# Optimization experiments

Hardware: AMD Instinct MI355X
Metric: run time of the kernel (lower is better)

## Reference

```python
import jax, jax.numpy as jnp
import numpy as np

B, S, D = 4, 4096, 256


def setup_inputs() -> dict:
    key = jax.random.key(0)
    k1, k2, k3 = jax.random.split(key, 3)
    x = jax.random.normal(k1, (B, S, D), dtype=jnp.float32)
    w_int = jax.random.randint(k2, (D, D), 0, 127, dtype=jnp.int32)  # quantized weight (out, in)
    scale = jax.random.uniform(k3, (D,), dtype=jnp.float32)          # per-output-channel scale
    return {"x": x, "w_int": w_int, "scale": scale}


def reference(x, w_int, scale):
    # self-attention: q = k = v = x, single head over feature dim D
    inv_sqrt_d = 1.0 / jnp.sqrt(jnp.asarray(D, dtype=x.dtype))
    scores = jnp.einsum('bqd,bkd->bqk', x, x) * inv_sqrt_d   # [B,S,S]
    probs = jax.nn.softmax(scores, axis=-1)
    attn = jnp.einsum('bqk,bkd->bqd', probs, x)              # [B,S,D]
    # quantized linear: dequantize then matmul (y = attn @ W^T)
    W = w_int.astype(x.dtype) * scale[:, None]               # [D_out, D_in]
    return jnp.einsum('bsd,od->bso', attn, W)
```

## Files before the change

### kernel.cpp

```cpp
#include <hip/hip_runtime.h>

typedef __bf16 bf16x8 __attribute__((ext_vector_type(8)));
typedef float f32x16 __attribute__((ext_vector_type(16)));
typedef unsigned short u16x8 __attribute__((ext_vector_type(8)));

constexpr int B = 4, S = 4096, D = 256;
constexpr float CSC = 0.09016844005556021f;

static __device__ __forceinline__ unsigned short f2bf(float f) {
  unsigned int u = __builtin_bit_cast(unsigned int, f);
  u = (u + 0x7fffu + ((u >> 16) & 1u)) >> 16;
  return (unsigned short)u;
}

static __device__ __forceinline__ float bf2f(unsigned short u) {
  unsigned int v = ((unsigned int)u) << 16;
  return __builtin_bit_cast(float, v);
}

static __device__ __forceinline__ unsigned int pk2bf(float lo, float hi) {
  unsigned int r;
  asm("v_cvt_pk_bf16_f32 %0, %1, %2" : "=v"(r) : "v"(lo), "v"(hi));
  return r;
}

static __device__ __forceinline__ void gld16(const void* g, void* l) {
  __builtin_amdgcn_global_load_lds(
      (const __attribute__((address_space(1))) unsigned int*)g,
      (__attribute__((address_space(3))) unsigned int*)l, 16, 0, 0);
}

#define FENCE_LGKM()                                          \
  do {                                                        \
    asm volatile("s_waitcnt lgkmcnt(0)" ::: "memory");        \
    __builtin_amdgcn_s_barrier();                             \
    asm volatile("" ::: "memory");                            \
  } while (0)
#define FENCE_ALL()                                               \
  do {                                                            \
    asm volatile("s_waitcnt vmcnt(0) lgkmcnt(0)" ::: "memory");   \
    __builtin_amdgcn_s_barrier();                                 \
    asm volatile("" ::: "memory");                                \
  } while (0)

__global__ __launch_bounds__(256) void k_prep(const float* __restrict__ x,
                                              unsigned short* __restrict__ xbf,
                                              unsigned short* __restrict__ xK,
                                              unsigned short* __restrict__ xV) {
  __shared__ unsigned short T[64][72];
  __shared__ unsigned short R[64][72];
  int bid = blockIdx.x;
  int b = bid >> 8, rem = bid & 255;
  int s0 = (rem >> 2) * 64, d0 = (rem & 3) * 64;
  int j = threadIdx.x & 63, i0 = threadIdx.x >> 6;
#pragma unroll
  for (int k = 0; k < 16; ++k) {
    int i = k * 4 + i0;
    int idx = (b * S + s0 + i) * D + d0 + j;
    unsigned short v = f2bf(x[idx]);
    xbf[idx] = v;
    T[j][i] = v;
    R[i][j] = v;
  }
  __syncthreads();
  int t = s0 >> 6;
#pragma unroll
  for (int p = 0; p < 2; ++p) {
    int cc = p * 256 + threadIdx.x;
    int i = cc >> 3;
    int sl = (cc >> 1) & 3;
    int half = cc & 1;
    u16x8 v = *(const u16x8*)&R[i][sl * 16 + half * 8];
    int s = (d0 >> 4) + sl;
    *(u16x8*)((char*)xK + (size_t)((b * 64 + t) * 16 + s) * 2048 + i * 32 + half * 16) = v;
  }
#pragma unroll
  for (int p = 0; p < 2; ++p) {
    int cc = p * 256 + threadIdx.x;
    int dl = cc >> 3;
    int p8 = cc & 7;
    u16x8 v = *(const u16x8*)&T[dl][p8 * 8];
    int c = p8 >> 1;
    *(u16x8*)((char*)xV + (size_t)((b * 64 + t) * 4 + c) * 8192 + (d0 + dl) * 32 +
              (p8 & 1) * 16) = v;
  }
}

__global__ __launch_bounds__(256) void k_deqw(const int* __restrict__ w,
                                              unsigned short* __restrict__ wbf) {
  int i = blockIdx.x * 256 + threadIdx.x;
  wbf[i] = f2bf((float)w[i]);
}

__global__ __launch_bounds__(512, 2) void k_attn(const unsigned short* __restrict__ xbf,
                                                 const unsigned short* __restrict__ xK,
                                                 const unsigned short* __restrict__ xV,
                                                 unsigned short* __restrict__ PO0,
                                                 unsigned short* __restrict__ PO1,
                                                 float* __restrict__ ML) {
  __shared__ __align__(16) char smem[147456];

  int tid = threadIdx.x;
  int w = tid >> 6, lane = tid & 63;
  int q5 = lane & 31, hi = lane >> 5;
  int pair = w >> 1, dh = w & 1;

  int bid = blockIdx.x;
  int swz = (bid & 7) * 32 + (bid >> 3);
  int h = swz & 1;
  int qg = swz >> 1;
  int q0 = qg * 128;
  int bat = q0 >> 12;
  int qloc = q0 & (S - 1);

  const unsigned short* Xb = xbf + (size_t)bat * (S * D);
  int qw = qloc + pair * 32;
  int koff = q5 * 32 + hi * 16;

  bf16x8 qf[16];
#pragma unroll
  for (int s = 0; s < 16; ++s)
    qf[s] = *(const bf16x8*)(Xb + (qw + q5) * D + s * 16 + hi * 8);

  f32x16 acc[4];
#pragma unroll
  for (int dt = 0; dt < 4; ++dt)
#pragma unroll
    for (int j = 0; j < 16; ++j) acc[dt][j] = 0.f;
  float l_lane = 0.f;

  const char* xKb = (const char*)xK + (size_t)(bat * 64 + h * 32) * 32768;
  const char* xVb = (const char*)xV + (size_t)(bat * 64 + h * 32) * 32768;

  auto STAGE = [&](int itile, int bb) {
    char* Kd = smem + bb * 32768;
    char* Vd = smem + 65536 + bb * 32768;
    const char* srcK = xKb + (size_t)itile * 32768;
    const char* srcV = xVb + (size_t)itile * 32768;
#pragma unroll
    for (int i = 0; i < 4; ++i) {
      int off = (w * 2 + (i >> 1)) * 2048 + (i & 1) * 1024;
      gld16(srcK + off + lane * 16, Kd + off);
    }
#pragma unroll
    for (int i = 0; i < 4; ++i) {
      int off = (w >> 1) * 8192 + ((w & 1) * 4 + i) * 1024;
      gld16(srcV + off + lane * 16, Vd + off);
    }
  };

  STAGE(0, 0);
  FENCE_ALL();

  char* Pb = smem + 131072 + pair * 4096;

  for (int it = 0; it < 32; ++it) {
    int bb = it & 1;
    if (it + 1 < 32) STAGE(it + 1, bb ^ 1);

    const char* Kt = smem + bb * 32768 + dh * 1024 + koff;
    f32x16 st;
#pragma unroll
    for (int j = 0; j < 16; ++j) st[j] = 0.f;
    __builtin_amdgcn_s_setprio(1);
#pragma unroll
    for (int s = 0; s < 16; ++s) {
      bf16x8 kf = *(const bf16x8*)(Kt + s * 2048);
      st = __builtin_amdgcn_mfma_f32_32x32x16_bf16(kf, qf[s], st, 0, 0, 0);
    }
    __builtin_amdgcn_s_setprio(0);

    float p[16];
    float ps = 0.f;
#pragma unroll
    for (int j = 0; j < 16; ++j) {
      p[j] = exp2f(st[j] * CSC);
      ps += p[j];
    }
    l_lane += ps;
    char* pw = Pb + dh * 2048 + q5 * 32 + hi * 8;
    {
      uint2 a = {pk2bf(p[0], p[1]), pk2bf(p[2], p[3])};
      uint2 b2 = {pk2bf(p[4], p[5]), pk2bf(p[6], p[7])};
      uint2 c2 = {pk2bf(p[8], p[9]), pk2bf(p[10], p[11])};
      uint2 d2 = {pk2bf(p[12], p[13]), pk2bf(p[14], p[15])};
      *(uint2*)(pw) = a;
      *(uint2*)(pw + 16) = b2;
      *(uint2*)(pw + 1024) = c2;
      *(uint2*)(pw + 1024 + 16) = d2;
    }
    FENCE_LGKM();

    const char* Vt = smem + 65536 + bb * 32768 + dh * 4096 + koff;
    const char* Pr = Pb + koff;
    __builtin_amdgcn_s_setprio(1);
#pragma unroll
    for (int s = 0; s < 4; ++s) {
      bf16x8 pa = *(const bf16x8*)(Pr + s * 1024);
#pragma unroll
      for (int dt = 0; dt < 4; ++dt) {
        bf16x8 vf = *(const bf16x8*)(Vt + s * 8192 + dt * 1024);
        acc[dt] = __builtin_amdgcn_mfma_f32_32x32x16_bf16(vf, pa, acc[dt], 0, 0, 0);
      }
    }
    __builtin_amdgcn_s_setprio(0);

    FENCE_ALL();
  }

  float lw = l_lane + __shfl_xor(l_lane, 32, 64);
  float* LX = (float*)(smem + 131072);
  if (lane < 32) LX[w * 32 + q5] = lw;
  __syncthreads();
  float l_tot = lw + LX[(w ^ 1) * 32 + q5];
  if (dh == 0 && lane < 32) {
    int row = q0 + pair * 32 + q5;
    ML[((size_t)h * 16384 + row) * 2 + 0] = 0.f;
    ML[((size_t)h * 16384 + row) * 2 + 1] = l_tot;
  }

  char* E = smem + w * 8704;
#pragma unroll
  for (int dt = 0; dt < 4; ++dt) {
#pragma unroll
    for (int a = 0; a < 4; ++a) {
      int dl = dt * 32 + 8 * a + 4 * hi;
      *(unsigned int*)(E + q5 * 272 + dl * 2) = pk2bf(acc[dt][4 * a + 0], acc[dt][4 * a + 1]);
      *(unsigned int*)(E + q5 * 272 + dl * 2 + 4) = pk2bf(acc[dt][4 * a + 2], acc[dt][4 * a + 3]);
    }
  }
  unsigned short* Pb2 = (h == 0) ? PO0 : PO1;
#pragma unroll
  for (int i = 0; i < 8; ++i) {
    int qr = i * 4 + (lane >> 4);
    int ch = lane & 15;
    u16x8 v = *(const u16x8*)(E + qr * 272 + ch * 16);
    *(u16x8*)(Pb2 + (size_t)(q0 + pair * 32 + qr) * 256 + dh * 128 + ch * 8) = v;
  }
}

__global__ __launch_bounds__(64) void k_gemm(const unsigned short* __restrict__ PO0,
                                             const unsigned short* __restrict__ PO1,
                                             const float* __restrict__ ML,
                                             const unsigned short* __restrict__ wbf,
                                             const float* __restrict__ scale,
                                             float* __restrict__ out) {
  int lane = threadIdx.x, g = lane >> 4, c = lane & 15;
  int m0 = blockIdx.x * 16;
  int o0 = blockIdx.y * 64;
  int row = m0 + c;
  float il = 1.f / (ML[(size_t)row * 2 + 1] + ML[((size_t)16384 + row) * 2 + 1]);
  union UU { uint4 u; bf16x8 v; };
  bf16x8 af[8];
#pragma unroll
  for (int dk = 0; dk < 8; ++dk) {
    u16x8 a0 = *(const u16x8*)(PO0 + (size_t)row * 256 + dk * 32 + g * 8);
    u16x8 a1 = *(const u16x8*)(PO1 + (size_t)row * 256 + dk * 32 + g * 8);
    UU cv;
#pragma unroll
    for (int e = 0; e < 4; ++e) {
      float lo = (bf2f(a0[2 * e]) + bf2f(a1[2 * e])) * il;
      float hi = (bf2f(a0[2 * e + 1]) + bf2f(a1[2 * e + 1])) * il;
      ((unsigned int*)&cv.u)[e] = pk2bf(lo, hi);
    }
    af[dk] = cv.v;
  }
  typedef float f32x4 __attribute__((ext_vector_type(4)));
  const f32x4 zero = {0.f, 0.f, 0.f, 0.f};
  f32x4 acc[4];
#pragma unroll
  for (int i = 0; i < 4; ++i) acc[i] = zero;
#pragma unroll
  for (int oc = 0; oc < 4; ++oc) {
#pragma unroll
    for (int dk = 0; dk < 8; ++dk) {
      bf16x8 wf = *(const bf16x8*)(wbf + (o0 + oc * 16 + c) * D + dk * 32 + g * 8);
      acc[oc] = __builtin_amdgcn_mfma_f32_16x16x32_bf16(af[dk], wf, acc[oc], 0, 0, 0);
    }
  }
#pragma unroll
  for (int oc = 0; oc < 4; ++oc) {
    float sc = scale[o0 + oc * 16 + c];
#pragma unroll
    for (int r = 0; r < 4; ++r)
      out[(m0 + 4 * g + r) * D + o0 + oc * 16 + c] = acc[oc][r] * sc;
  }
}

extern "C" void kernel_launch(void* const* d_in, const int* in_sizes, int n_in,
                              void* d_out, int out_size, void* d_ws, size_t ws_size,
                              hipStream_t stream) {
  (void)in_sizes; (void)n_in; (void)out_size; (void)ws_size;
  const float* x = (const float*)d_in[0];
  const int* w_int = (const int*)d_in[1];
  const float* scale = (const float*)d_in[2];
  float* out = (float*)d_out;

  char* ws = (char*)d_ws;
  unsigned short* xbf = (unsigned short*)(ws);
  unsigned short* xK  = (unsigned short*)(ws + 8388608);
  unsigned short* xV  = (unsigned short*)(ws + 16777216);
  unsigned short* wbf = (unsigned short*)(ws + 25165824);
  float*          ML  = (float*)(ws + 25296896);
  unsigned short* PO0 = (unsigned short*)(ws + 25821184);
  unsigned short* PO1 = (unsigned short*)(ws + 34209792);

  k_prep<<<dim3(1024), dim3(256), 0, stream>>>(x, xbf, xK, xV);
  k_deqw<<<dim3(256), dim3(256), 0, stream>>>(w_int, wbf);
  k_attn<<<dim3(256), dim3(512), 0, stream>>>(xbf, xK, xV, PO0, PO1, ML);
  k_gemm<<<dim3(1024, 4), dim3(64), 0, stream>>>(PO0, PO1, ML, wbf, scale, out);
}
```

Baseline: 118.1 us.

## Keep P in registers via permlane32 swap and split PV over key halves

```diff
diff --git a/kernel.cpp b/kernel.cpp
--- a/kernel.cpp
+++ b/kernel.cpp
@@ -30,12 +30,6 @@
       (__attribute__((address_space(3))) unsigned int*)l, 16, 0, 0);
 }
 
-#define FENCE_LGKM()                                          \
-  do {                                                        \
-    asm volatile("s_waitcnt lgkmcnt(0)" ::: "memory");        \
-    __builtin_amdgcn_s_barrier();                             \
-    asm volatile("" ::: "memory");                            \
-  } while (0)
 #define FENCE_ALL()                                               \
   do {                                                            \
     asm volatile("s_waitcnt vmcnt(0) lgkmcnt(0)" ::: "memory");   \
@@ -98,7 +92,7 @@
                                                  unsigned short* __restrict__ PO0,
                                                  unsigned short* __restrict__ PO1,
                                                  float* __restrict__ ML) {
-  __shared__ __align__(16) char smem[147456];
+  __shared__ __align__(16) char smem[132096];
 
   int tid = threadIdx.x;
   int w = tid >> 6, lane = tid & 63;
@@ -122,9 +116,9 @@
   for (int s = 0; s < 16; ++s)
     qf[s] = *(const bf16x8*)(Xb + (qw + q5) * D + s * 16 + hi * 8);
 
-  f32x16 acc[4];
-#pragma unroll
-  for (int dt = 0; dt < 4; ++dt)
+  f32x16 acc[8];
+#pragma unroll
+  for (int dt = 0; dt < 8; ++dt)
 #pragma unroll
     for (int j = 0; j < 16; ++j) acc[dt][j] = 0.f;
   float l_lane = 0.f;
@@ -152,8 +146,6 @@
   STAGE(0, 0);
   FENCE_ALL();
 
-  char* Pb = smem + 131072 + pair * 4096;
-
   for (int it = 0; it < 32; ++it) {
     int bb = it & 1;
     if (it + 1 < 32) STAGE(it + 1, bb ^ 1);
@@ -170,36 +162,38 @@
     }
     __builtin_amdgcn_s_setprio(0);
 
-    float p[16];
+    unsigned int pk[8];
     float ps = 0.f;
 #pragma unroll
-    for (int j = 0; j < 16; ++j) {
-      p[j] = exp2f(st[j] * CSC);
-      ps += p[j];
+    for (int a = 0; a < 8; ++a) {
+      float lo = exp2f(st[2 * a] * CSC);
+      float hh = exp2f(st[2 * a + 1] * CSC);
+      ps += lo + hh;
+      pk[a] = pk2bf(lo, hh);
     }
     l_lane += ps;
-    char* pw = Pb + dh * 2048 + q5 * 32 + hi * 8;
-    {
-      uint2 a = {pk2bf(p[0], p[1]), pk2bf(p[2], p[3])};
-      uint2 b2 = {pk2bf(p[4], p[5]), pk2bf(p[6], p[7])};
-      uint2 c2 = {pk2bf(p[8], p[9]), pk2bf(p[10], p[11])};
-      uint2 d2 = {pk2bf(p[12], p[13]), pk2bf(p[14], p[15])};
-      *(uint2*)(pw) = a;
-      *(uint2*)(pw + 16) = b2;
-      *(uint2*)(pw + 1024) = c2;
-      *(uint2*)(pw + 1024 + 16) = d2;
-    }
-    FENCE_LGKM();
-
-    const char* Vt = smem + 65536 + bb * 32768 + dh * 4096 + koff;
-    const char* Pr = Pb + koff;
+
+    unsigned int a0 = pk[0], b0 = pk[2];
+    unsigned int a1 = pk[1], b1 = pk[3];
+    unsigned int a2 = pk[4], b2 = pk[6];
+    unsigned int a3 = pk[5], b3 = pk[7];
+    asm volatile("v_permlane32_swap_b32 %0, %1" : "+v"(a0), "+v"(b0));
+    asm volatile("v_permlane32_swap_b32 %0, %1" : "+v"(a1), "+v"(b1));
+    asm volatile("v_permlane32_swap_b32 %0, %1" : "+v"(a2), "+v"(b2));
+    asm volatile("v_permlane32_swap_b32 %0, %1" : "+v"(a3), "+v"(b3));
+    union PA { unsigned int u[4]; bf16x8 v; };
+    PA pa0, pa1;
+    pa0.u[0] = a0; pa0.u[1] = a1; pa0.u[2] = b0; pa0.u[3] = b1;
+    pa1.u[0] = a2; pa1.u[1] = a3; pa1.u[2] = b2; pa1.u[3] = b3;
+
     __builtin_amdgcn_s_setprio(1);
 #pragma unroll
-    for (int s = 0; s < 4; ++s) {
-      bf16x8 pa = *(const bf16x8*)(Pr + s * 1024);
-#pragma unroll
-      for (int dt = 0; dt < 4; ++dt) {
-        bf16x8 vf = *(const bf16x8*)(Vt + s * 8192 + dt * 1024);
+    for (int s2i = 0; s2i < 2; ++s2i) {
+      const char* Vt = smem + 65536 + bb * 32768 + (dh * 2 + s2i) * 8192 + koff;
+      bf16x8 pa = (s2i == 0) ? pa0.v : pa1.v;
+#pragma unroll
+      for (int dt = 0; dt < 8; ++dt) {
+        bf16x8 vf = *(const bf16x8*)(Vt + dt * 1024);
         acc[dt] = __builtin_amdgcn_mfma_f32_32x32x16_bf16(vf, pa, acc[dt], 0, 0, 0);
       }
     }
@@ -218,24 +212,53 @@
     ML[((size_t)h * 16384 + row) * 2 + 0] = 0.f;
     ML[((size_t)h * 16384 + row) * 2 + 1] = l_tot;
   }
-
-  char* E = smem + w * 8704;
-#pragma unroll
-  for (int dt = 0; dt < 4; ++dt) {
-#pragma unroll
-    for (int a = 0; a < 4; ++a) {
-      int dl = dt * 32 + 8 * a + 4 * hi;
-      *(unsigned int*)(E + q5 * 272 + dl * 2) = pk2bf(acc[dt][4 * a + 0], acc[dt][4 * a + 1]);
-      *(unsigned int*)(E + q5 * 272 + dl * 2 + 4) = pk2bf(acc[dt][4 * a + 2], acc[dt][4 * a + 3]);
-    }
-  }
+  __syncthreads();
+
   unsigned short* Pb2 = (h == 0) ? PO0 : PO1;
 #pragma unroll
-  for (int i = 0; i < 8; ++i) {
-    int qr = i * 4 + (lane >> 4);
-    int ch = lane & 15;
-    u16x8 v = *(const u16x8*)(E + qr * 272 + ch * 16);
-    *(u16x8*)(Pb2 + (size_t)(q0 + pair * 32 + qr) * 256 + dh * 128 + ch * 8) = v;
+  for (int rh = 0; rh < 2; ++rh) {
+    float* slot = (float*)(smem + w * 16384);
+#pragma unroll
+    for (int dt4 = 0; dt4 < 4; ++dt4) {
+#pragma unroll
+      for (int r = 0; r < 16; ++r) {
+        int dloc = dt4 * 32 + (r & 3) + 8 * (r >> 2) + 4 * hi;
+        slot[dloc * 32 + q5] = acc[rh * 4 + dt4][r];
+      }
+    }
+    __syncthreads();
+    if (dh == rh) {
+      const float* pslot = (const float*)(smem + (w ^ 1) * 16384);
+#pragma unroll
+      for (int dt4 = 0; dt4 < 4; ++dt4) {
+#pragma unroll
+        for (int r = 0; r < 16; ++r) {
+          int dloc = dt4 * 32 + (r & 3) + 8 * (r >> 2) + 4 * hi;
+          acc[rh * 4 + dt4][r] += pslot[dloc * 32 + q5];
+        }
+      }
+      char* E = smem + w * 16384;
+#pragma unroll
+      for (int dt4 = 0; dt4 < 4; ++dt4) {
+#pragma unroll
+        for (int a = 0; a < 4; ++a) {
+          int dl = dt4 * 32 + 8 * a + 4 * hi;
+          *(unsigned int*)(E + q5 * 272 + dl * 2) =
+              pk2bf(acc[rh * 4 + dt4][4 * a + 0], acc[rh * 4 + dt4][4 * a + 1]);
+          *(unsigned int*)(E + q5 * 272 + dl * 2 + 4) =
+              pk2bf(acc[rh * 4 + dt4][4 * a + 2], acc[rh * 4 + dt4][4 * a + 3]);
+        }
+      }
+      asm volatile("s_waitcnt lgkmcnt(0)" ::: "memory");
+#pragma unroll
+      for (int i = 0; i < 8; ++i) {
+        int qr = i * 4 + (lane >> 4);
+        int ch = lane & 15;
+        u16x8 v = *(const u16x8*)(E + qr * 272 + ch * 16);
+        *(u16x8*)(Pb2 + (size_t)(q0 + pair * 32 + qr) * 256 + rh * 128 + ch * 8) = v;
+      }
+    }
+    __syncthreads();
   }
 }
 
```

Result: no change. 116.7 us (-1.1%).
